# Kernel tuning notes

Measured on AMD Instinct MI355X. Metric: run time of the kernel, lower is better.

Reference implementation:

```python
import jax, jax.numpy as jnp
import numpy as np

N = 50000   # nodes
E = 800000  # edges per order
F = 128     # input features (== hidden so layers stack)
H = 128     # hidden
C = 10      # classes
L = 3       # num_layers
O = 2       # Order (max_petal_dim)
K = 10      # propagation hops
G = 128     # num graphs in batch
ALPHA = 0.5
EPS = 1e-5  # BatchNorm eps


def _fw_init():
    # HiGCN_prop.reset_parameters: fW[k] = alpha*(1-alpha)^k, fW[K] = (1-alpha)^K
    fw = np.array([ALPHA * (1 - ALPHA) ** k for k in range(K + 1)], dtype=np.float32)
    fw[-1] = (1 - ALPHA) ** K
    return jnp.broadcast_to(jnp.asarray(fw), (L, O, K + 1))


def setup_inputs() -> dict:
    key = jax.random.key(0)
    ks = iter(jax.random.split(key, 64))
    nk = lambda: next(ks)
    s = lambda shape: (jax.random.normal(nk(), shape, jnp.float32) * 0.05)
    x = jax.random.normal(nk(), (N, F), jnp.float32)
    edge_index = jax.random.randint(nk(), (O, 2, E), 0, N, dtype=jnp.int32)
    # scale weights so expected row sum ~0.5 -> stable over K=10 hops
    edge_weight = jax.random.uniform(nk(), (O, E), jnp.float32) * (1.0 / 16.0)
    batch = jnp.sort(jax.random.randint(nk(), (N,), 0, G, dtype=jnp.int32))
    return {
        "x": x, "edge_index": edge_index, "edge_weight": edge_weight, "batch": batch,
        "W_in": s((L, O, F, H)), "b_in": s((L, O, H)),
        "fW": _fw_init(),
        "W_out": s((L, O * H, H)), "b_out": s((L, H)),
        "Wn1": s((L, H, H)), "bn1": s((L, H)), "g1": jnp.ones((L, H), jnp.float32), "be1": s((L, H)),
        "Wn2": s((L, H, H)), "bn2": s((L, H)), "g2": jnp.ones((L, H), jnp.float32), "be2": s((L, H)),
        "W1": s((H, H)), "b1": s((H,)), "W2": s((H, C)), "b2": s((C,)),
    }


def _bn(x, g, b):
    # eval-mode BatchNorm1d: running_mean=0, running_var=1
    return x * (g / jnp.sqrt(1.0 + EPS)) + b


def _spmm(dst, src, w, h):
    # out[dst] += w * h[src]  == matmul(HL, h, reduce='add')
    return jax.ops.segment_sum(w[:, None] * h[src], dst, num_segments=N)


def reference(x, edge_index, edge_weight, batch, W_in, b_in, fW, W_out, b_out,
              Wn1, bn1, g1, be1, Wn2, bn2, g2, be2, W1, b1, W2, b2):
    h = x
    for l in range(L):
        outs = []
        for o in range(O):
            dst, src = edge_index[o, 0], edge_index[o, 1]
            w = edge_weight[o]
            z = h @ W_in[l, o] + b_in[l, o]           # [N, H]
            hid = fW[l, o, 0] * z
            for k in range(K):
                z = _spmm(dst, src, w, z)
                hid = hid + fW[l, o, k + 1] * z
            outs.append(hid)
        xc = jnp.concatenate(outs, axis=1) @ W_out[l] + b_out[l]   # [N, H]
        xc = jnp.maximum(_bn(xc @ Wn1[l] + bn1[l], g1[l], be1[l]), 0.0)
        h = jnp.maximum(_bn(xc @ Wn2[l] + bn2[l], g2[l], be2[l]), 0.0)
    p = jax.ops.segment_sum(h, batch, num_segments=G)              # global_add_pool [G, H]
    p = jnp.maximum(p @ W1 + b1, 0.0)
    return p @ W2 + b2                                             # [G, C]
```

## Files before the change

kernel.cpp:

```cpp
#include <hip/hip_runtime.h>

#define NNODES 50000
#define NEDGES 800000
#define HDIM 128
#define CDIM 10
#define LNUM 3
#define ONUM 2
#define KHOPS 10
#define GNUM 128
#define EPSBN 1e-5f

typedef unsigned int uint;
typedef unsigned short ushort;
typedef __attribute__((ext_vector_type(8))) short bf16x8;
typedef __attribute__((ext_vector_type(4))) float f32x4;

__device__ __forceinline__ ushort f2bf(float f) {
    uint u = __builtin_bit_cast(uint, f);
    uint r = (u + 0x7fffu + ((u >> 16) & 1u)) >> 16;
    return (ushort)r;
}
__device__ __forceinline__ float bf2f_lo(uint u) { return __builtin_bit_cast(float, u << 16); }
__device__ __forceinline__ float bf2f_hi(uint u) { return __builtin_bit_cast(float, u & 0xffff0000u); }

#define KC 128
#define LDA 136
__global__ __launch_bounds__(256) void mfma_gemm(
    const float* __restrict__ A0, const float* __restrict__ A1,
    const ushort* __restrict__ Wt, int Kdim,
    const float* __restrict__ bias, const float* __restrict__ g,
    const float* __restrict__ be, const float* __restrict__ fw0,
    float* __restrict__ outf, ushort* __restrict__ outz,
    float* __restrict__ hid, int relu,
    const ushort* __restrict__ Wt_b, const float* __restrict__ bias_b,
    const float* __restrict__ fw0_b, ushort* __restrict__ outz_b,
    float* __restrict__ hid_b)
{
    if (blockIdx.y) { Wt = Wt_b; bias = bias_b; fw0 = fw0_b; outz = outz_b; hid = hid_b; }
    __shared__ ushort sA[64 * LDA];
    __shared__ ushort sB[128 * LDA];
    const int row0 = blockIdx.x * 64;
    const int tid  = threadIdx.x;
    const int w    = tid >> 6;
    const int lane = tid & 63;
    const int lr   = lane & 15;
    const int q    = lane >> 4;

    f32x4 acc[8];
#pragma unroll
    for (int nt = 0; nt < 8; ++nt)
#pragma unroll
        for (int j = 0; j < 4; ++j) acc[nt][j] = 0.f;

    const int nch = A1 ? 2 : 1;
    for (int c = 0; c < nch; ++c) {
        const float* Asrc = c ? A1 : A0;
        for (int idx = tid; idx < 64 * 64; idx += 256) {
            int r = idx >> 6, kp = idx & 63;
            int row = row0 + r;
            float2 v = make_float2(0.f, 0.f);
            if (row < NNODES) v = ((const float2*)(Asrc + (size_t)row * HDIM))[kp];
            uint pv = (uint)f2bf(v.x) | ((uint)f2bf(v.y) << 16);
            ((uint*)(sA + r * LDA))[kp] = pv;
        }
        for (int idx = tid; idx < 128 * 64; idx += 256) {
            int n = idx >> 6, kp = idx & 63;
            uint u = ((const uint*)(Wt + (size_t)n * Kdim + c * KC))[kp];
            ((uint*)(sB + n * LDA))[kp] = u;
        }
        __syncthreads();
#pragma unroll
        for (int kt = 0; kt < 4; ++kt) {
            bf16x8 a = *(const bf16x8*)(sA + (16 * w + lr) * LDA + kt * 32 + q * 8);
#pragma unroll
            for (int nt = 0; nt < 8; ++nt) {
                bf16x8 b = *(const bf16x8*)(sB + (nt * 16 + lr) * LDA + kt * 32 + q * 8);
                acc[nt] = __builtin_amdgcn_mfma_f32_16x16x32_bf16(a, b, acc[nt], 0, 0, 0);
            }
        }
        __syncthreads();
    }

    const float f0 = fw0 ? fw0[0] : 0.f;
#pragma unroll
    for (int nt = 0; nt < 8; ++nt) {
        int col = nt * 16 + lr;
        float bs = bias[col];
        float sc = 1.f, bt = 0.f;
        if (g) { sc = g[col] * rsqrtf(1.f + EPSBN); bt = be[col]; }
#pragma unroll
        for (int r = 0; r < 4; ++r) {
            int row = row0 + 16 * w + q * 4 + r;
            if (row >= NNODES) continue;
            float v = acc[nt][r] + bs;
            if (g) v = v * sc + bt;
            if (relu) v = fmaxf(v, 0.f);
            size_t off = (size_t)row * HDIM + col;
            if (outf) outf[off] = v;
            if (outz) outz[off] = f2bf(v);
            if (hid)  hid[off]  = f0 * v;
        }
    }
}

__global__ void wtrans_all(const float* __restrict__ W_in, const float* __restrict__ W_out,
                           const float* __restrict__ Wn1, const float* __restrict__ Wn2,
                           ushort* __restrict__ Wt_in, ushort* __restrict__ Wt_out,
                           ushort* __restrict__ Wt_n1, ushort* __restrict__ Wt_n2)
{
    int b = blockIdx.x;
    const float* W; ushort* Wt; int Kd;
    if (b < 6)       { Kd = HDIM;     W = W_in  + (size_t)b * Kd * HDIM;        Wt = Wt_in  + (size_t)b * Kd * HDIM; }
    else if (b < 9)  { Kd = 2 * HDIM; W = W_out + (size_t)(b - 6) * Kd * HDIM;  Wt = Wt_out + (size_t)(b - 6) * Kd * HDIM; }
    else if (b < 12) { Kd = HDIM;     W = Wn1   + (size_t)(b - 9) * Kd * HDIM;  Wt = Wt_n1  + (size_t)(b - 9) * Kd * HDIM; }
    else             { Kd = HDIM;     W = Wn2   + (size_t)(b - 12) * Kd * HDIM; Wt = Wt_n2  + (size_t)(b - 12) * Kd * HDIM; }
    for (int idx = threadIdx.x; idx < Kd * HDIM; idx += 512) {
        int k = idx >> 7, n = idx & 127;
        Wt[(size_t)n * Kd + k] = f2bf(W[idx]);
    }
}

__global__ void gemm_rows(const float* __restrict__ A0,
                          const float* __restrict__ W, const float* __restrict__ bias,
                          float* __restrict__ out, int N, int Hout, int relu)
{
    __shared__ float a[8][HDIM];
    const int row0 = blockIdx.x * 8;
    const int tid  = threadIdx.x;
    for (int r = 0; r < 8; ++r) {
        int row = row0 + r;
        a[r][tid] = (row < N) ? A0[(size_t)row * HDIM + tid] : 0.f;
    }
    __syncthreads();
    if (tid < Hout) {
        float acc[8];
#pragma unroll
        for (int r = 0; r < 8; ++r) acc[r] = 0.f;
        for (int k = 0; k < HDIM; ++k) {
            float wv = W[(size_t)k * Hout + tid];
#pragma unroll
            for (int r = 0; r < 8; ++r) acc[r] += a[r][k] * wv;
        }
        const float bs = bias[tid];
        for (int r = 0; r < 8; ++r) {
            int row = row0 + r;
            if (row >= N) break;
            float v = acc[r] + bs;
            if (relu) v = fmaxf(v, 0.f);
            out[(size_t)row * Hout + tid] = v;
        }
    }
}

__global__ void fill2(const int* __restrict__ ei, const float* __restrict__ ew,
                      int* __restrict__ cnt0, int* __restrict__ cnt1,
                      uint* __restrict__ bk0, uint* __restrict__ bk1)
{
    int e = blockIdx.x * blockDim.x + threadIdx.x;
    if (e >= NEDGES) return;
    int o = blockIdx.y;
    const int* dst = ei + (size_t)o * 2 * NEDGES;
    const int* src = dst + NEDGES;
    float w = ew[(size_t)o * NEDGES + e];
    int d = dst[e];
    int pos = atomicAdd((o ? cnt1 : cnt0) + d, 1);
    if (pos < 64)
        (o ? bk1 : bk0)[((size_t)d << 6) + pos] = ((uint)f2bf(w) << 16) | (uint)src[e];
}

__global__ void spmm2(const int* __restrict__ cnt0, const uint* __restrict__ bk0,
                      const int* __restrict__ cnt1, const uint* __restrict__ bk1,
                      const ushort* __restrict__ zin0, ushort* __restrict__ zout0,
                      const ushort* __restrict__ zin1, ushort* __restrict__ zout1,
                      float* __restrict__ hid0, float* __restrict__ hid1,
                      const float* __restrict__ fw0p, const float* __restrict__ fw1p,
                      int do_hid)
{
    const int node = blockIdx.x * 4 + (threadIdx.x >> 6);
    if (node >= NNODES) return;
    const int o    = blockIdx.y;
    const int lane = threadIdx.x & 63;
    const int*  cnt = o ? cnt1 : cnt0;
    const uint* bk  = o ? bk1 : bk0;
    const uint* zi  = (const uint*)(o ? zin1 : zin0);
    uint*       zo  = (uint*)(o ? zout1 : zout0);
    float*      hid = o ? hid1 : hid0;
    const float* fwp = o ? fw1p : fw0p;

    int n = cnt[node]; n = n > 64 ? 64 : n;
    const uint* b = bk + ((size_t)node << 6);
    float ax = 0.f, ay = 0.f;
    int j = 0;
    for (; j + 3 < n; j += 4) {
        uint4 e4 = *(const uint4*)(b + j);
        uint u0 = zi[(size_t)(e4.x & 0xffffu) * 64 + lane];
        uint u1 = zi[(size_t)(e4.y & 0xffffu) * 64 + lane];
        uint u2 = zi[(size_t)(e4.z & 0xffffu) * 64 + lane];
        uint u3 = zi[(size_t)(e4.w & 0xffffu) * 64 + lane];
        float w0 = bf2f_hi(e4.x), w1 = bf2f_hi(e4.y);
        float w2 = bf2f_hi(e4.z), w3 = bf2f_hi(e4.w);
        ax += w0 * bf2f_lo(u0) + w1 * bf2f_lo(u1) + w2 * bf2f_lo(u2) + w3 * bf2f_lo(u3);
        ay += w0 * bf2f_hi(u0) + w1 * bf2f_hi(u1) + w2 * bf2f_hi(u2) + w3 * bf2f_hi(u3);
    }
    for (; j < n; ++j) {
        uint e = b[j];
        uint u = zi[(size_t)(e & 0xffffu) * 64 + lane];
        float wt = bf2f_hi(e);
        ax += wt * bf2f_lo(u);
        ay += wt * bf2f_hi(u);
    }
    zo[(size_t)node * 64 + lane] = (uint)f2bf(ax) | ((uint)f2bf(ay) << 16);
    if (do_hid) {
        uint up = zi[(size_t)node * 64 + lane];
        const float c0 = fwp[0], c1 = fwp[1];
        float2* hp = (float2*)hid + (size_t)node * 64 + lane;
        float2 h = *hp;
        h.x += c0 * bf2f_lo(up) + c1 * ax;
        h.y += c0 * bf2f_hi(up) + c1 * ay;
        *hp = h;
    }
}

__global__ __launch_bounds__(1024) void pool_seg(const float* __restrict__ h,
                                                 const int* __restrict__ batch,
                                                 float* __restrict__ pool)
{
    __shared__ float red[1024];
    const int gph = blockIdx.x;
    const int t  = threadIdx.x & 127;
    const int rr = threadIdx.x >> 7;
    int lo = 0, hi = NNODES;
    while (lo < hi) { int m = (lo + hi) >> 1; if (batch[m] < gph) lo = m + 1; else hi = m; }
    const int beg = lo;
    hi = NNODES;
    while (lo < hi) { int m = (lo + hi) >> 1; if (batch[m] < gph + 1) lo = m + 1; else hi = m; }
    const int end = lo;
    float acc = 0.f;
    for (int i = beg + rr; i < end; i += 8) acc += h[(size_t)i * HDIM + t];
    red[threadIdx.x] = acc;
    __syncthreads();
    if (rr == 0) {
        float s = 0.f;
#pragma unroll
        for (int k = 0; k < 8; ++k) s += red[t + 128 * k];
        pool[(size_t)gph * HDIM + t] = s;
    }
}

extern "C" void kernel_launch(void* const* d_in, const int* in_sizes, int n_in,
                              void* d_out, int out_size, void* d_ws, size_t ws_size,
                              hipStream_t stream)
{
    const float* x     = (const float*)d_in[0];
    const int*   ei    = (const int*)  d_in[1];
    const float* ew    = (const float*)d_in[2];
    const int*   batch = (const int*)  d_in[3];
    const float* W_in  = (const float*)d_in[4];
    const float* b_in  = (const float*)d_in[5];
    const float* fW    = (const float*)d_in[6];
    const float* W_out = (const float*)d_in[7];
    const float* b_out = (const float*)d_in[8];
    const float* Wn1   = (const float*)d_in[9];
    const float* bn1   = (const float*)d_in[10];
    const float* g1    = (const float*)d_in[11];
    const float* be1   = (const float*)d_in[12];
    const float* Wn2   = (const float*)d_in[13];
    const float* bn2   = (const float*)d_in[14];
    const float* g2    = (const float*)d_in[15];
    const float* be2   = (const float*)d_in[16];
    const float* W1    = (const float*)d_in[17];
    const float* b1    = (const float*)d_in[18];
    const float* W2    = (const float*)d_in[19];
    const float* b2    = (const float*)d_in[20];
    float* out = (float*)d_out;

    const size_t NH = (size_t)NNODES * HDIM;
    float* ws  = (float*)d_ws;
    float*  f_A = ws;
    float*  f_B = ws + NH;
    ushort* z0A = (ushort*)(ws + 2 * NH);
    ushort* z0B = z0A + NH;
    ushort* z1A = z0B + NH;
    ushort* z1B = z1A + NH;
    float*  f_pl  = (float*)(z1B + NH);
    float*  f_pl2 = f_pl + (size_t)GNUM * HDIM;

    ushort* Wt_in  = (ushort*)(f_pl2 + (size_t)GNUM * HDIM);
    ushort* Wt_out = Wt_in  + (size_t)6 * HDIM * HDIM;
    ushort* Wt_n1  = Wt_out + (size_t)3 * 2 * HDIM * HDIM;
    ushort* Wt_n2  = Wt_n1  + (size_t)3 * HDIM * HDIM;

    int*  cnt0 = (int*)(Wt_n2 + (size_t)3 * HDIM * HDIM);
    int*  cnt1 = cnt0 + NNODES;
    uint* bk0  = (uint*)(cnt1 + NNODES);
    uint* bk1  = bk0 + ((size_t)NNODES << 6);

    const int gemm_grid = (NNODES + 63) / 64;
    const int edge_grid = (NEDGES + 255) / 256;
    const dim3 spmm_grid((NNODES + 3) / 4, 2);

    wtrans_all<<<15, 512, 0, stream>>>(W_in, W_out, Wn1, Wn2, Wt_in, Wt_out, Wt_n1, Wt_n2);
    hipMemsetAsync(cnt0, 0, 2 * NNODES * sizeof(int), stream);
    fill2<<<dim3(edge_grid, 2), 256, 0, stream>>>(ei, ew, cnt0, cnt1, bk0, bk1);

    const float* curH = x;
    for (int l = 0; l < LNUM; ++l) {
        float* h0 = (curH == (const float*)f_A) ? f_B : f_A;
        float* h1 = (l == 0) ? f_B : (float*)curH;
        const int lo0 = l * ONUM, lo1 = lo0 + 1;
        mfma_gemm<<<dim3(gemm_grid, 2), 256, 0, stream>>>(
            curH, nullptr, Wt_in + (size_t)lo0 * HDIM * HDIM, HDIM,
            b_in + (size_t)lo0 * HDIM, nullptr, nullptr,
            fW + (size_t)lo0 * (KHOPS + 1), nullptr, z0A, h0, 0,
            Wt_in + (size_t)lo1 * HDIM * HDIM, b_in + (size_t)lo1 * HDIM,
            fW + (size_t)lo1 * (KHOPS + 1), z1A, h1);

        ushort *pa0 = z0A, *pb0 = z0B, *pa1 = z1A, *pb1 = z1B;
        for (int k = 1; k <= KHOPS; ++k) {
            spmm2<<<spmm_grid, 256, 0, stream>>>(
                cnt0, bk0, cnt1, bk1, pa0, pb0, pa1, pb1, h0, h1,
                fW + (size_t)lo0 * (KHOPS + 1) + (k - 1),
                fW + (size_t)lo1 * (KHOPS + 1) + (k - 1),
                (k & 1) == 0);
            ushort* t;
            t = pa0; pa0 = pb0; pb0 = t;
            t = pa1; pa1 = pb1; pb1 = t;
        }
        mfma_gemm<<<gemm_grid, 256, 0, stream>>>(
            h0, h1, Wt_out + (size_t)l * 2 * HDIM * HDIM, 2 * HDIM,
            b_out + (size_t)l * HDIM, nullptr, nullptr, nullptr,
            h0, nullptr, nullptr, 0,
            nullptr, nullptr, nullptr, nullptr, nullptr);
        mfma_gemm<<<gemm_grid, 256, 0, stream>>>(
            h0, nullptr, Wt_n1 + (size_t)l * HDIM * HDIM, HDIM,
            bn1 + (size_t)l * HDIM, g1 + (size_t)l * HDIM, be1 + (size_t)l * HDIM,
            nullptr, h1, nullptr, nullptr, 1,
            nullptr, nullptr, nullptr, nullptr, nullptr);
        mfma_gemm<<<gemm_grid, 256, 0, stream>>>(
            h1, nullptr, Wt_n2 + (size_t)l * HDIM * HDIM, HDIM,
            bn2 + (size_t)l * HDIM, g2 + (size_t)l * HDIM, be2 + (size_t)l * HDIM,
            nullptr, h0, nullptr, nullptr, 1,
            nullptr, nullptr, nullptr, nullptr, nullptr);
        curH = h0;
    }

    pool_seg<<<GNUM, 1024, 0, stream>>>(curH, batch, f_pl);
    gemm_rows<<<(GNUM + 7) / 8, 128, 0, stream>>>(f_pl,  W1, b1, f_pl2, GNUM, HDIM, 1);
    gemm_rows<<<(GNUM + 7) / 8, 128, 0, stream>>>(f_pl2, W2, b2, out,   GNUM, CDIM, 0);
}
```

Before: 2.896 ms.

## Fold W_out into Wn1 and store hidden activations as bf16

Precomputes the product W_out·Wn1 and its folded bias on the device, which removes one GEMM launch per layer because there is no nonlinearity between those two linear layers. The hidden accumulators and the intermediate node features move from fp32 to bf16, halving their read and write traffic in the spmm hop kernels and the GEMMs, with a three-buffer rotation for the activations. It also uses readfirstlane on the edge count so it is held in a scalar register. The cost is extra bf16 rounding in the running hop accumulation and in the folded weights.

```diff
diff --git a/kernel.cpp b/kernel.cpp
--- a/kernel.cpp
+++ b/kernel.cpp
@@ -26,17 +26,16 @@
 #define KC 128
 #define LDA 136
 __global__ __launch_bounds__(256) void mfma_gemm(
-    const float* __restrict__ A0, const float* __restrict__ A1,
+    const void* __restrict__ A0, const void* __restrict__ A1, int a_bf16,
     const ushort* __restrict__ Wt, int Kdim,
     const float* __restrict__ bias, const float* __restrict__ g,
     const float* __restrict__ be, const float* __restrict__ fw0,
-    float* __restrict__ outf, ushort* __restrict__ outz,
-    float* __restrict__ hid, int relu,
+    ushort* __restrict__ outz, ushort* __restrict__ hidz, int relu,
     const ushort* __restrict__ Wt_b, const float* __restrict__ bias_b,
     const float* __restrict__ fw0_b, ushort* __restrict__ outz_b,
-    float* __restrict__ hid_b)
-{
-    if (blockIdx.y) { Wt = Wt_b; bias = bias_b; fw0 = fw0_b; outz = outz_b; hid = hid_b; }
+    ushort* __restrict__ hidz_b)
+{
+    if (blockIdx.y) { Wt = Wt_b; bias = bias_b; fw0 = fw0_b; outz = outz_b; hidz = hidz_b; }
     __shared__ ushort sA[64 * LDA];
     __shared__ ushort sB[128 * LDA];
     const int row0 = blockIdx.x * 64;
@@ -54,13 +53,19 @@
 
     const int nch = A1 ? 2 : 1;
     for (int c = 0; c < nch; ++c) {
-        const float* Asrc = c ? A1 : A0;
+        const void* Asrc = c ? A1 : A0;
         for (int idx = tid; idx < 64 * 64; idx += 256) {
             int r = idx >> 6, kp = idx & 63;
             int row = row0 + r;
-            float2 v = make_float2(0.f, 0.f);
-            if (row < NNODES) v = ((const float2*)(Asrc + (size_t)row * HDIM))[kp];
-            uint pv = (uint)f2bf(v.x) | ((uint)f2bf(v.y) << 16);
+            uint pv = 0;
+            if (row < NNODES) {
+                if (a_bf16) {
+                    pv = ((const uint*)((const ushort*)Asrc + (size_t)row * HDIM))[kp];
+                } else {
+                    float2 v = ((const float2*)((const float*)Asrc + (size_t)row * HDIM))[kp];
+                    pv = (uint)f2bf(v.x) | ((uint)f2bf(v.y) << 16);
+                }
+            }
             ((uint*)(sA + r * LDA))[kp] = pv;
         }
         for (int idx = tid; idx < 128 * 64; idx += 256) {
@@ -96,27 +101,45 @@
             if (g) v = v * sc + bt;
             if (relu) v = fmaxf(v, 0.f);
             size_t off = (size_t)row * HDIM + col;
-            if (outf) outf[off] = v;
             if (outz) outz[off] = f2bf(v);
-            if (hid)  hid[off]  = f0 * v;
-        }
-    }
-}
-
-__global__ void wtrans_all(const float* __restrict__ W_in, const float* __restrict__ W_out,
-                           const float* __restrict__ Wn1, const float* __restrict__ Wn2,
-                           ushort* __restrict__ Wt_in, ushort* __restrict__ Wt_out,
-                           ushort* __restrict__ Wt_n1, ushort* __restrict__ Wt_n2)
+            if (hidz) hidz[off] = f2bf(f0 * v);
+        }
+    }
+}
+
+__global__ void wtrans_all(const float* __restrict__ W_in, const float* __restrict__ Wn2,
+                           ushort* __restrict__ Wt_in, ushort* __restrict__ Wt_n2)
 {
     int b = blockIdx.x;
-    const float* W; ushort* Wt; int Kd;
-    if (b < 6)       { Kd = HDIM;     W = W_in  + (size_t)b * Kd * HDIM;        Wt = Wt_in  + (size_t)b * Kd * HDIM; }
-    else if (b < 9)  { Kd = 2 * HDIM; W = W_out + (size_t)(b - 6) * Kd * HDIM;  Wt = Wt_out + (size_t)(b - 6) * Kd * HDIM; }
-    else if (b < 12) { Kd = HDIM;     W = Wn1   + (size_t)(b - 9) * Kd * HDIM;  Wt = Wt_n1  + (size_t)(b - 9) * Kd * HDIM; }
-    else             { Kd = HDIM;     W = Wn2   + (size_t)(b - 12) * Kd * HDIM; Wt = Wt_n2  + (size_t)(b - 12) * Kd * HDIM; }
-    for (int idx = threadIdx.x; idx < Kd * HDIM; idx += 512) {
+    const float* W; ushort* Wt;
+    if (b < 6) { W = W_in + (size_t)b * HDIM * HDIM;       Wt = Wt_in + (size_t)b * HDIM * HDIM; }
+    else       { W = Wn2 + (size_t)(b - 6) * HDIM * HDIM;  Wt = Wt_n2 + (size_t)(b - 6) * HDIM * HDIM; }
+    for (int idx = threadIdx.x; idx < HDIM * HDIM; idx += 512) {
         int k = idx >> 7, n = idx & 127;
-        Wt[(size_t)n * Kd + k] = f2bf(W[idx]);
+        Wt[(size_t)n * HDIM + k] = f2bf(W[idx]);
+    }
+}
+
+__global__ void wfold(const float* __restrict__ W_out, const float* __restrict__ b_out,
+                      const float* __restrict__ Wn1, const float* __restrict__ bn1,
+                      ushort* __restrict__ Wt_fold, float* __restrict__ b_fold)
+{
+    const int l = blockIdx.y, bx = blockIdx.x;
+    const float* Wo = W_out + (size_t)l * 2 * HDIM * HDIM;
+    const float* Wn = Wn1   + (size_t)l * HDIM * HDIM;
+    const int n = threadIdx.x & 127;
+    const int j = threadIdx.x >> 7;
+#pragma unroll
+    for (int t = 0; t < 2; ++t) {
+        int kk = bx * 4 + j * 2 + t;
+        float s = 0.f;
+        for (int m = 0; m < HDIM; ++m) s += Wo[(size_t)kk * HDIM + m] * Wn[(size_t)m * HDIM + n];
+        Wt_fold[(size_t)l * HDIM * 2 * HDIM + (size_t)n * 2 * HDIM + kk] = f2bf(s);
+    }
+    if (bx == 0 && j == 0) {
+        float s = bn1[(size_t)l * HDIM + n];
+        for (int m = 0; m < HDIM; ++m) s += b_out[(size_t)l * HDIM + m] * Wn[(size_t)m * HDIM + n];
+        b_fold[(size_t)l * HDIM + n] = s;
     }
 }
 
@@ -172,7 +195,7 @@
                       const int* __restrict__ cnt1, const uint* __restrict__ bk1,
                       const ushort* __restrict__ zin0, ushort* __restrict__ zout0,
                       const ushort* __restrict__ zin1, ushort* __restrict__ zout1,
-                      float* __restrict__ hid0, float* __restrict__ hid1,
+                      ushort* __restrict__ hid0, ushort* __restrict__ hid1,
                       const float* __restrict__ fw0p, const float* __restrict__ fw1p,
                       int do_hid)
 {
@@ -184,10 +207,10 @@
     const uint* bk  = o ? bk1 : bk0;
     const uint* zi  = (const uint*)(o ? zin1 : zin0);
     uint*       zo  = (uint*)(o ? zout1 : zout0);
-    float*      hid = o ? hid1 : hid0;
+    uint*       hid = (uint*)(o ? hid1 : hid0);
     const float* fwp = o ? fw1p : fw0p;
 
-    int n = cnt[node]; n = n > 64 ? 64 : n;
+    int n = __builtin_amdgcn_readfirstlane(cnt[node]); n = n > 64 ? 64 : n;
     const uint* b = bk + ((size_t)node << 6);
     float ax = 0.f, ay = 0.f;
     int j = 0;
@@ -212,16 +235,15 @@
     zo[(size_t)node * 64 + lane] = (uint)f2bf(ax) | ((uint)f2bf(ay) << 16);
     if (do_hid) {
         uint up = zi[(size_t)node * 64 + lane];
+        uint hh = hid[(size_t)node * 64 + lane];
         const float c0 = fwp[0], c1 = fwp[1];
-        float2* hp = (float2*)hid + (size_t)node * 64 + lane;
-        float2 h = *hp;
-        h.x += c0 * bf2f_lo(up) + c1 * ax;
-        h.y += c0 * bf2f_hi(up) + c1 * ay;
-        *hp = h;
-    }
-}
-
-__global__ __launch_bounds__(1024) void pool_seg(const float* __restrict__ h,
+        float hx = bf2f_lo(hh) + c0 * bf2f_lo(up) + c1 * ax;
+        float hy = bf2f_hi(hh) + c0 * bf2f_hi(up) + c1 * ay;
+        hid[(size_t)node * 64 + lane] = (uint)f2bf(hx) | ((uint)f2bf(hy) << 16);
+    }
+}
+
+__global__ __launch_bounds__(1024) void pool_seg(const ushort* __restrict__ h,
                                                  const int* __restrict__ batch,
                                                  float* __restrict__ pool)
 {
@@ -236,7 +258,8 @@
     while (lo < hi) { int m = (lo + hi) >> 1; if (batch[m] < gph + 1) lo = m + 1; else hi = m; }
     const int end = lo;
     float acc = 0.f;
-    for (int i = beg + rr; i < end; i += 8) acc += h[(size_t)i * HDIM + t];
+    for (int i = beg + rr; i < end; i += 8)
+        acc += __builtin_bit_cast(float, (uint)h[(size_t)i * HDIM + t] << 16);
     red[threadIdx.x] = acc;
     __syncthreads();
     if (rr == 0) {
@@ -275,22 +298,21 @@
     float* out = (float*)d_out;
 
     const size_t NH = (size_t)NNODES * HDIM;
-    float* ws  = (float*)d_ws;
-    float*  f_A = ws;
-    float*  f_B = ws + NH;
-    ushort* z0A = (ushort*)(ws + 2 * NH);
+    ushort* wsu = (ushort*)d_ws;
+    ushort* nb[3] = { wsu, wsu + NH, wsu + 2 * NH };
+    ushort* z0A = wsu + 3 * NH;
     ushort* z0B = z0A + NH;
     ushort* z1A = z0B + NH;
     ushort* z1B = z1A + NH;
     float*  f_pl  = (float*)(z1B + NH);
     float*  f_pl2 = f_pl + (size_t)GNUM * HDIM;
-
-    ushort* Wt_in  = (ushort*)(f_pl2 + (size_t)GNUM * HDIM);
-    ushort* Wt_out = Wt_in  + (size_t)6 * HDIM * HDIM;
-    ushort* Wt_n1  = Wt_out + (size_t)3 * 2 * HDIM * HDIM;
-    ushort* Wt_n2  = Wt_n1  + (size_t)3 * HDIM * HDIM;
-
-    int*  cnt0 = (int*)(Wt_n2 + (size_t)3 * HDIM * HDIM);
+    float*  b_fold = f_pl2 + (size_t)GNUM * HDIM;
+
+    ushort* Wt_in   = (ushort*)(b_fold + 3 * HDIM);
+    ushort* Wt_n2   = Wt_in + (size_t)6 * HDIM * HDIM;
+    ushort* Wt_fold = Wt_n2 + (size_t)3 * HDIM * HDIM;
+
+    int*  cnt0 = (int*)(Wt_fold + (size_t)3 * HDIM * 2 * HDIM);
     int*  cnt1 = cnt0 + NNODES;
     uint* bk0  = (uint*)(cnt1 + NNODES);
     uint* bk1  = bk0 + ((size_t)NNODES << 6);
@@ -299,26 +321,31 @@
     const int edge_grid = (NEDGES + 255) / 256;
     const dim3 spmm_grid((NNODES + 3) / 4, 2);
 
-    wtrans_all<<<15, 512, 0, stream>>>(W_in, W_out, Wn1, Wn2, Wt_in, Wt_out, Wt_n1, Wt_n2);
+    wtrans_all<<<9, 512, 0, stream>>>(W_in, Wn2, Wt_in, Wt_n2);
+    wfold<<<dim3(64, 3), 256, 0, stream>>>(W_out, b_out, Wn1, bn1, Wt_fold, b_fold);
     hipMemsetAsync(cnt0, 0, 2 * NNODES * sizeof(int), stream);
     fill2<<<dim3(edge_grid, 2), 256, 0, stream>>>(ei, ew, cnt0, cnt1, bk0, bk1);
 
-    const float* curH = x;
+    int ci = -1;
     for (int l = 0; l < LNUM; ++l) {
-        float* h0 = (curH == (const float*)f_A) ? f_B : f_A;
-        float* h1 = (l == 0) ? f_B : (float*)curH;
+        const int t0 = (l == 0) ? 0 : (ci + 1) % 3;
+        const int t1 = (l == 0) ? 1 : (ci + 2) % 3;
+        const int cx = (l == 0) ? 2 : ci;
+        const void* curp = (l == 0) ? (const void*)x : (const void*)nb[ci];
+        const int a_bf = (l == 0) ? 0 : 1;
         const int lo0 = l * ONUM, lo1 = lo0 + 1;
+
         mfma_gemm<<<dim3(gemm_grid, 2), 256, 0, stream>>>(
-            curH, nullptr, Wt_in + (size_t)lo0 * HDIM * HDIM, HDIM,
+            curp, nullptr, a_bf, Wt_in + (size_t)lo0 * HDIM * HDIM, HDIM,
             b_in + (size_t)lo0 * HDIM, nullptr, nullptr,
-            fW + (size_t)lo0 * (KHOPS + 1), nullptr, z0A, h0, 0,
+            fW + (size_t)lo0 * (KHOPS + 1), z0A, nb[t0], 0,
             Wt_in + (size_t)lo1 * HDIM * HDIM, b_in + (size_t)lo1 * HDIM,
-            fW + (size_t)lo1 * (KHOPS + 1), z1A, h1);
+            fW + (size_t)lo1 * (KHOPS + 1), z1A, nb[t1]);
 
         ushort *pa0 = z0A, *pb0 = z0B, *pa1 = z1A, *pb1 = z1B;
         for (int k = 1; k <= KHOPS; ++k) {
             spmm2<<<spmm_grid, 256, 0, stream>>>(
-                cnt0, bk0, cnt1, bk1, pa0, pb0, pa1, pb1, h0, h1,
+                cnt0, bk0, cnt1, bk1, pa0, pb0, pa1, pb1, nb[t0], nb[t1],
                 fW + (size_t)lo0 * (KHOPS + 1) + (k - 1),
                 fW + (size_t)lo1 * (KHOPS + 1) + (k - 1),
                 (k & 1) == 0);
@@ -327,24 +354,19 @@
             t = pa1; pa1 = pb1; pb1 = t;
         }
         mfma_gemm<<<gemm_grid, 256, 0, stream>>>(
-            h0, h1, Wt_out + (size_t)l * 2 * HDIM * HDIM, 2 * HDIM,
-            b_out + (size_t)l * HDIM, nullptr, nullptr, nullptr,
-            h0, nullptr, nullptr, 0,
+            nb[t0], nb[t1], 1, Wt_fold + (size_t)l * HDIM * 2 * HDIM, 2 * HDIM,
+            b_fold + (size_t)l * HDIM, g1 + (size_t)l * HDIM, be1 + (size_t)l * HDIM,
+            nullptr, nb[cx], nullptr, 1,
             nullptr, nullptr, nullptr, nullptr, nullptr);
         mfma_gemm<<<gemm_grid, 256, 0, stream>>>(
-            h0, nullptr, Wt_n1 + (size_t)l * HDIM * HDIM, HDIM,
-            bn1 + (size_t)l * HDIM, g1 + (size_t)l * HDIM, be1 + (size_t)l * HDIM,
-            nullptr, h1, nullptr, nullptr, 1,
+            nb[cx], nullptr, 1, Wt_n2 + (size_t)l * HDIM * HDIM, HDIM,
+            bn2 + (size_t)l * HDIM, g2 + (size_t)l * HDIM, be2 + (size_t)l * HDIM,
+            nullptr, nb[t0], nullptr, 1,
             nullptr, nullptr, nullptr, nullptr, nullptr);
-        mfma_gemm<<<gemm_grid, 256, 0, stream>>>(
-            h1, nullptr, Wt_n2 + (size_t)l * HDIM * HDIM, HDIM,
-            bn2 + (size_t)l * HDIM, g2 + (size_t)l * HDIM, be2 + (size_t)l * HDIM,
-            nullptr, h0, nullptr, nullptr, 1,
-            nullptr, nullptr, nullptr, nullptr, nullptr);
-        curH = h0;
-    }
-
-    pool_seg<<<GNUM, 1024, 0, stream>>>(curH, batch, f_pl);
+        ci = t0;
+    }
+
+    pool_seg<<<GNUM, 1024, 0, stream>>>(nb[ci], batch, f_pl);
     gemm_rows<<<(GNUM + 7) / 8, 128, 0, stream>>>(f_pl,  W1, b1, f_pl2, GNUM, HDIM, 1);
     gemm_rows<<<(GNUM + 7) / 8, 128, 0, stream>>>(f_pl2, W2, b2, out,   GNUM, CDIM, 0);
 }
```

Result: faster. 2.728 ms (-5.8%).
